# Performance work log

Measured on AMD Instinct MI355X. Metric: run time of the kernel, lower is better.

## Reference

```python
import jax, jax.numpy as jnp
import numpy as np

NEG_SLOPE = 0.2  # PyG GATConv default negative_slope


def gat_conv(x, edge_index, W, att_src, att_dst, bias):
    """PyG-style GATConv (concat heads, add_self_loops=True, eval mode).
    x: [N, F_in], edge_index: [2, E] (row 0 = src j, row 1 = dst i).
    W: [F_in, H*C], att_src/att_dst: [H, C], bias: [H*C].
    """
    N = x.shape[0]
    H, C = att_src.shape
    loops = jnp.arange(N, dtype=edge_index.dtype)
    src = jnp.concatenate([edge_index[0], loops])  # [E+N]
    dst = jnp.concatenate([edge_index[1], loops])
    h = (x @ W).reshape(N, H, C)                              # [N,H,C]
    a_src = jnp.einsum('nhc,hc->nh', h, att_src)              # [N,H]
    a_dst = jnp.einsum('nhc,hc->nh', h, att_dst)
    alpha = jax.nn.leaky_relu(a_src[src] + a_dst[dst], NEG_SLOPE)  # [E+N,H]
    # segment softmax over edges sharing the same destination node
    m = jax.ops.segment_max(alpha, dst, num_segments=N)       # [N,H]
    e = jnp.exp(alpha - jax.lax.stop_gradient(m)[dst])
    denom = jax.ops.segment_sum(e, dst, num_segments=N)       # [N,H]
    a = e / (denom[dst] + 1e-16)                              # [E+N,H]
    msg = h[src] * a[:, :, None]                              # [E+N,H,C]
    out = jax.ops.segment_sum(msg, dst, num_segments=N)       # [N,H,C]
    return out.reshape(N, H * C) + bias


def setup_inputs() -> dict:
    key = jax.random.key(0)
    ks = jax.random.split(key, 10)
    N, F, NC, C1, H1 = 50000, 128, 40, 16, 8
    E = 800000
    x = jax.random.normal(ks[0], (N, F), dtype=jnp.float32)
    edge_index = jax.random.randint(ks[1], (2, E), 0, N, dtype=jnp.int64)
    s1 = 1.0 / np.sqrt(F)
    W1 = jax.random.uniform(ks[2], (F, H1 * C1), jnp.float32, -s1, s1)
    att_src1 = jax.random.uniform(ks[3], (H1, C1), jnp.float32, -1.0, 1.0) * s1
    att_dst1 = jax.random.uniform(ks[4], (H1, C1), jnp.float32, -1.0, 1.0) * s1
    bias1 = jnp.zeros((H1 * C1,), jnp.float32)
    s2 = 1.0 / np.sqrt(H1 * C1)
    W2 = jax.random.uniform(ks[5], (H1 * C1, NC), jnp.float32, -s2, s2)
    att_src2 = jax.random.uniform(ks[6], (1, NC), jnp.float32, -1.0, 1.0) * s2
    att_dst2 = jax.random.uniform(ks[7], (1, NC), jnp.float32, -1.0, 1.0) * s2
    bias2 = jnp.zeros((NC,), jnp.float32)
    return {"x": x, "edge_index": edge_index, "W1": W1, "att_src1": att_src1,
            "att_dst1": att_dst1, "bias1": bias1, "W2": W2, "att_src2": att_src2,
            "att_dst2": att_dst2, "bias2": bias2}


def reference(x, edge_index, W1, att_src1, att_dst1, bias1, W2, att_src2, att_dst2, bias2):
    h = gat_conv(x, edge_index, W1, att_src1, att_dst1, bias1)   # [N, 128]
    # dropout in eval mode = identity
    out = gat_conv(h, edge_index, W2, att_src2, att_dst2, bias2)  # [N, 40]
    return out
```

## Files before the change

### kernel.cpp

```cpp
#include <hip/hip_runtime.h>
#include <hip/hip_bf16.h>
#include <math.h>

#define NEG_SLOPE 0.2f

typedef __bf16 bf16x8 __attribute__((ext_vector_type(8)));
typedef float f32x4 __attribute__((ext_vector_type(4)));

__device__ __forceinline__ float lrelu(float x) { return x > 0.f ? x : NEG_SLOPE * x; }

__device__ __forceinline__ unsigned short f2bfu(float f) {
    unsigned int ua = __float_as_uint(f);
    return (unsigned short)((ua + 0x7fffu + ((ua >> 16) & 1u)) >> 16);
}
__device__ __forceinline__ float bfu2f(unsigned short u) {
    return __uint_as_float(((unsigned int)u) << 16);
}
__device__ __forceinline__ float bf_lo(unsigned int u) { return __uint_as_float(u << 16); }
__device__ __forceinline__ float bf_hi(unsigned int u) { return __uint_as_float(u & 0xffff0000u); }

__global__ __launch_bounds__(256) void k_prep(const float* __restrict__ W1,
                                              bf16x8* __restrict__ Wp,
                                              const float* __restrict__ W2,
                                              bf16x8* __restrict__ W2p,
                                              int* __restrict__ cnt, int N) {
    int g = blockIdx.x * 256 + threadIdx.x;
    if (g < 2048) {
        int n = g & 15, quad = (g >> 4) & 3, c = (g >> 6) & 3, ct = g >> 8;
        bf16x8 v;
#pragma unroll
        for (int j = 0; j < 8; ++j)
            v[j] = (__bf16)W1[(c * 32 + quad * 8 + j) * 128 + ct * 16 + n];
        Wp[g] = v;
    } else if (g < 2816) {
        int idx = g - 2048;
        int n = idx & 15, quad = (idx >> 4) & 3, c = (idx >> 6) & 3, ct = idx >> 8;
        int colc = ct * 16 + n;
        bf16x8 v;
#pragma unroll
        for (int j = 0; j < 8; ++j)
            v[j] = (colc < 40) ? (__bf16)W2[(c * 32 + quad * 8 + j) * 40 + colc] : (__bf16)0.f;
        W2p[idx] = v;
    }
    if (g < N) cnt[g] = 0;
}

__global__ __launch_bounds__(256) void k_hist(const int* __restrict__ ei, int E, int N,
                                              int* __restrict__ cnt,
                                              unsigned short* __restrict__ rank) {
    int e = blockIdx.x * 256 + threadIdx.x;
    if (e >= E + N) return;
    int d = (e < E) ? ei[E + e] : (e - E);
    rank[e] = (unsigned short)atomicAdd(&cnt[d], 1);
}

__global__ __launch_bounds__(256) void k_scan_part(const int* __restrict__ cnt, int N,
                                                   int* __restrict__ psum) {
    __shared__ int sh[256];
    int t = threadIdx.x;
    int base = blockIdx.x * 1024 + t * 4;
    int tl = 0;
#pragma unroll
    for (int j = 0; j < 4; ++j) tl += (base + j < N) ? cnt[base + j] : 0;
    sh[t] = tl; __syncthreads();
    for (int off = 128; off > 0; off >>= 1) {
        if (t < off) sh[t] += sh[t + off];
        __syncthreads();
    }
    if (t == 0) psum[blockIdx.x] = sh[0];
}

__global__ __launch_bounds__(256) void k_scan_add(const int* __restrict__ cnt, int N,
                                                  const int* __restrict__ psum,
                                                  int* __restrict__ rowptr) {
    __shared__ int sh[256];
    __shared__ int basep;
    int t = threadIdx.x;
    if (t == 0) {
        int s = 0;
        for (int i = 0; i < blockIdx.x; ++i) s += psum[i];
        basep = s;
    }
    int base = blockIdx.x * 1024 + t * 4;
    int c[4]; int tl = 0;
#pragma unroll
    for (int j = 0; j < 4; ++j) { c[j] = (base + j < N) ? cnt[base + j] : 0; tl += c[j]; }
    sh[t] = tl; __syncthreads();
    for (int off = 1; off < 256; off <<= 1) {
        int a = (t >= off) ? sh[t - off] : 0;
        __syncthreads();
        sh[t] += a;
        __syncthreads();
    }
    int run = basep + (sh[t] - tl);
#pragma unroll
    for (int j = 0; j < 4; ++j) {
        if (base + j < N) { rowptr[base + j] = run; run += c[j]; }
    }
}

__global__ __launch_bounds__(256) void k_scatter(const int* __restrict__ ei, int E, int N,
                                                 const int* __restrict__ rowptr,
                                                 const unsigned short* __restrict__ rank,
                                                 unsigned short* __restrict__ col) {
    int e = blockIdx.x * 256 + threadIdx.x;
    if (e >= E + N) return;
    int s, d;
    if (e < E) { s = ei[e]; d = ei[E + e]; } else { s = d = e - E; }
    col[rowptr[d] + (int)rank[e]] = (unsigned short)s;
}

__global__ __launch_bounds__(256) void k_gemm1(const float* __restrict__ x,
                                               const bf16x8* __restrict__ Wp,
                                               const float* __restrict__ att_s,
                                               const float* __restrict__ att_d,
                                               unsigned short* __restrict__ h1A,
                                               unsigned short* __restrict__ h1B,
                                               float* __restrict__ a_src,
                                               float* __restrict__ a_dst, int N) {
    int t = threadIdx.x;
    int w = t >> 6, lane = t & 63, quad = lane >> 4, n16 = lane & 15;
    int row0 = blockIdx.x * 64 + w * 16;
    int arow = row0 + n16; if (arow >= N) arow = N - 1;
    const float* px = x + (size_t)arow * 128;

    bf16x8 ah[4], al[4];
#pragma unroll
    for (int c = 0; c < 4; ++c) {
        float4 v0 = *(const float4*)&px[c * 32 + quad * 8];
        float4 v1 = *(const float4*)&px[c * 32 + quad * 8 + 4];
        float xf[8] = {v0.x, v0.y, v0.z, v0.w, v1.x, v1.y, v1.z, v1.w};
#pragma unroll
        for (int j = 0; j < 8; ++j) {
            __bf16 hi = (__bf16)xf[j];
            ah[c][j] = hi;
            al[c][j] = (__bf16)(xf[j] - (float)hi);
        }
    }

    f32x4 acc[8];
#pragma unroll
    for (int ct = 0; ct < 8; ++ct) acc[ct] = (f32x4){0.f, 0.f, 0.f, 0.f};

    const uint4* wp4 = (const uint4*)Wp;
#pragma unroll
    for (int ct = 0; ct < 8; ++ct) {
#pragma unroll
        for (int c = 0; c < 4; ++c) {
            union { uint4 u; bf16x8 b; } bu;
            bu.u = wp4[((ct * 4 + c) * 4 + quad) * 16 + n16];
            acc[ct] = __builtin_amdgcn_mfma_f32_16x16x32_bf16(ah[c], bu.b, acc[ct], 0, 0, 0);
            acc[ct] = __builtin_amdgcn_mfma_f32_16x16x32_bf16(al[c], bu.b, acc[ct], 0, 0, 0);
        }
    }

    float asv[8], adv[8];
#pragma unroll
    for (int ct = 0; ct < 8; ++ct) {
        asv[ct] = att_s[ct * 16 + n16];
        adv[ct] = att_d[ct * 16 + n16];
    }
    int nodeb = row0 + quad * 4;
#pragma unroll
    for (int ct = 0; ct < 8; ++ct) {
        unsigned short* hp = (ct < 4) ? h1A : h1B;
        int chl = (ct & 3) * 16 + n16;
#pragma unroll
        for (int reg = 0; reg < 4; ++reg) {
            int node = nodeb + reg;
            float hv = acc[ct][reg];
            float ps = hv * asv[ct];
            float pd = hv * adv[ct];
#pragma unroll
            for (int m = 1; m < 16; m <<= 1) {
                ps += __shfl_xor(ps, m);
                pd += __shfl_xor(pd, m);
            }
            if (node < N) {
                hp[(size_t)node * 64 + chl] = f2bfu(hv);
                if (n16 == 0) {
                    a_src[(size_t)node * 8 + ct] = ps;
                    a_dst[(size_t)node * 8 + ct] = pd;
                }
            }
        }
    }
}

__global__ __launch_bounds__(256) void k_aggr1(const int* __restrict__ rowptr,
                                               const int* __restrict__ cnt,
                                               const unsigned short* __restrict__ col,
                                               const float* __restrict__ a_src,
                                               const float* __restrict__ a_dst,
                                               const unsigned int* __restrict__ h1A,
                                               const unsigned int* __restrict__ h1B,
                                               const float* __restrict__ bias1,
                                               unsigned int* __restrict__ out1h,
                                               unsigned int* __restrict__ out1l,
                                               int N, int nag) {
    __shared__ float evs[4][2][128];
    __shared__ int   cls[4][2][32];
    int p = (blockIdx.x >= nag) ? 1 : 0;
    int blk = blockIdx.x - p * nag;
    const unsigned int* hp = p ? h1B : h1A;
    int t = threadIdx.x;
    int w = t >> 6;
    int lane = t & 63;
    int half = lane >> 5;
    int u = lane & 31;
    int node = blk * 8 + w * 2 + half;
    bool nv = (node < N);
    int nodec = nv ? node : (N - 1);
    int beg = rowptr[nodec];
    int deg = nv ? cnt[nodec] : 0;
    int degO = __shfl_xor(deg, 32);
    int degmax = (deg > degO) ? deg : degO;
    if (degmax <= 0) return;

    int hh = u >> 3;
    float4 ad4 = *(const float4*)&a_dst[(size_t)nodec * 8 + p * 4];

    float* myev = &evs[w][half][0];
    int*   mycl = &cls[w][half][0];

    float den = 0.f, n0 = 0.f, n1 = 0.f;
    int c = 0;
    while (c < degmax) {
        int slot = c + u;
        int slotc = (slot < deg) ? slot : (deg - 1);
        if (slotc < 0) slotc = 0;
        int su = (int)col[beg + slotc];
        float4 as4 = *(const float4*)&a_src[(size_t)su * 8 + p * 4];
        bool valid = (slot < deg);
        float e0 = valid ? __expf(lrelu(as4.x + ad4.x)) : 0.f;
        float e1 = valid ? __expf(lrelu(as4.y + ad4.y)) : 0.f;
        float e2 = valid ? __expf(lrelu(as4.z + ad4.z)) : 0.f;
        float e3 = valid ? __expf(lrelu(as4.w + ad4.w)) : 0.f;
        *(float4*)&myev[u * 4] = make_float4(e0, e1, e2, e3);
        mycl[u] = su;

        int ccm = degmax - c; ccm = (ccm < 32) ? ccm : 32;
        int last = ccm - 1;
        int s0 = mycl[0];
        unsigned int u0 = hp[s0 * 32 + u];
        int i1 = (1 < last) ? 1 : last;
        int s1 = mycl[i1];
        unsigned int u1 = hp[s1 * 32 + u];
        int i2 = (2 < last) ? 2 : last;
        int s2 = mycl[i2];
        unsigned int u2 = hp[s2 * 32 + u];
        int body = ccm - 3;
        int i = 0;
#pragma unroll 4
        for (; i < body; ++i) {
            int sN = mycl[i + 3];
            unsigned int uN = hp[sN * 32 + u];
            float ev = myev[i * 4 + hh];
            den += ev;
            n0 = fmaf(ev, bf_lo(u0), n0);
            n1 = fmaf(ev, bf_hi(u0), n1);
            u0 = u1; u1 = u2; u2 = uN;
        }
        for (; i < ccm; ++i) {
            float ev = myev[i * 4 + hh];
            den += ev;
            n0 = fmaf(ev, bf_lo(u0), n0);
            n1 = fmaf(ev, bf_hi(u0), n1);
            u0 = u1; u1 = u2;
        }
        c += 32;
    }
    if (nv) {
        float inv = 1.f / (den + 1e-16f);
        int ch = p * 64 + 2 * u;
        float2 b = *(const float2*)&bias1[ch];
        float o0 = fmaf(n0, inv, b.x), o1 = fmaf(n1, inv, b.y);
        unsigned short h0 = f2bfu(o0), h1 = f2bfu(o1);
        float l0 = o0 - bfu2f(h0), l1 = o1 - bfu2f(h1);
        size_t idx = (size_t)node * 64 + p * 32 + u;
        out1h[idx] = (unsigned int)h0 | ((unsigned int)h1 << 16);
        out1l[idx] = (unsigned int)f2bfu(l0) | ((unsigned int)f2bfu(l1) << 16);
    }
}

__global__ __launch_bounds__(256) void k_gemm2(const unsigned int* __restrict__ out1h,
                                               const unsigned int* __restrict__ out1l,
                                               const bf16x8* __restrict__ W2p,
                                               const float* __restrict__ att_s2,
                                               const float* __restrict__ att_d2,
                                               unsigned short* __restrict__ h2s,
                                               float* __restrict__ a_src2,
                                               float* __restrict__ a_dst2, int N) {
    int t = threadIdx.x;
    int w = t >> 6, lane = t & 63, quad = lane >> 4, n16 = lane & 15;
    int row0 = blockIdx.x * 64 + w * 16;
    int arow = row0 + n16; if (arow >= N) arow = N - 1;

    bf16x8 ah[4], al[4];
#pragma unroll
    for (int c = 0; c < 4; ++c) {
        size_t base = (size_t)arow * 64 + (c * 32 + quad * 8) / 2;
        union { uint4 u; bf16x8 b; } hu, lu;
        hu.u = *(const uint4*)&out1h[base];
        lu.u = *(const uint4*)&out1l[base];
        ah[c] = hu.b;
        al[c] = lu.b;
    }

    f32x4 acc[3];
#pragma unroll
    for (int ct = 0; ct < 3; ++ct) acc[ct] = (f32x4){0.f, 0.f, 0.f, 0.f};

    const uint4* wp4 = (const uint4*)W2p;
#pragma unroll
    for (int ct = 0; ct < 3; ++ct) {
#pragma unroll
        for (int c = 0; c < 4; ++c) {
            union { uint4 u; bf16x8 b; } bu;
            bu.u = wp4[((ct * 4 + c) * 4 + quad) * 16 + n16];
            acc[ct] = __builtin_amdgcn_mfma_f32_16x16x32_bf16(ah[c], bu.b, acc[ct], 0, 0, 0);
            acc[ct] = __builtin_amdgcn_mfma_f32_16x16x32_bf16(al[c], bu.b, acc[ct], 0, 0, 0);
        }
    }

    float asv[3], adv[3];
#pragma unroll
    for (int ct = 0; ct < 3; ++ct) {
        int ch = ct * 16 + n16;
        asv[ct] = (ch < 40) ? att_s2[ch] : 0.f;
        adv[ct] = (ch < 40) ? att_d2[ch] : 0.f;
    }
    int nodeb = row0 + quad * 4;
#pragma unroll
    for (int reg = 0; reg < 4; ++reg) {
        int node = nodeb + reg;
        float ps = 0.f, pd = 0.f;
#pragma unroll
        for (int ct = 0; ct < 3; ++ct) {
            float hv = acc[ct][reg];
            ps = fmaf(hv, asv[ct], ps);
            pd = fmaf(hv, adv[ct], pd);
            int ch = ct * 16 + n16;
            if (node < N && ch < 40) h2s[(size_t)node * 64 + ch] = f2bfu(hv);
        }
#pragma unroll
        for (int m = 1; m < 16; m <<= 1) {
            ps += __shfl_xor(ps, m);
            pd += __shfl_xor(pd, m);
        }
        if (node < N && n16 == 0) {
            a_src2[node] = ps;
            a_dst2[node] = pd;
        }
    }
}

__global__ __launch_bounds__(256) void k_aggr2(const int* __restrict__ rowptr,
                                               const int* __restrict__ cnt,
                                               const unsigned short* __restrict__ col,
                                               const float* __restrict__ a_src,
                                               const float* __restrict__ a_dst,
                                               const unsigned int* __restrict__ h2b,
                                               const float* __restrict__ bias2,
                                               float* __restrict__ out, int N) {
    __shared__ float evs[4][2][32];
    __shared__ int   cls[4][2][32];
    int t = threadIdx.x;
    int w = t >> 6;
    int lane = t & 63;
    int half = lane >> 5;
    int u = lane & 31;
    int node = blockIdx.x * 8 + w * 2 + half;
    bool nv = (node < N);
    int nodec = nv ? node : (N - 1);
    int beg = rowptr[nodec];
    int deg = nv ? cnt[nodec] : 0;
    int degO = __shfl_xor(deg, 32);
    int degmax = (deg > degO) ? deg : degO;
    if (degmax <= 0) return;

    int ucl = (u < 20) ? u : 19;
    float ad = a_dst[nodec];
    float* myev = &evs[w][half][0];
    int*   mycl = &cls[w][half][0];

    float den = 0.f, a0 = 0.f, a1 = 0.f;
    int c = 0;
    while (c < degmax) {
        int slot = c + u;
        int slotc = (slot < deg) ? slot : (deg - 1);
        if (slotc < 0) slotc = 0;
        int su = (int)col[beg + slotc];
        float ev = (slot < deg) ? __expf(lrelu(a_src[su] + ad)) : 0.f;
        myev[u] = ev;
        mycl[u] = su;

        int ccm = degmax - c; ccm = (ccm < 32) ? ccm : 32;
        int last = ccm - 1;
        int s0 = mycl[0];
        unsigned int u0 = h2b[s0 * 32 + ucl];
        int i1 = (1 < last) ? 1 : last;
        int s1 = mycl[i1];
        unsigned int u1 = h2b[s1 * 32 + ucl];
        int i2 = (2 < last) ? 2 : last;
        int s2 = mycl[i2];
        unsigned int u2 = h2b[s2 * 32 + ucl];
        int body = ccm - 3;
        int i = 0;
#pragma unroll 4
        for (; i < body; ++i) {
            int sN = mycl[i + 3];
            unsigned int uN = h2b[sN * 32 + ucl];
            float evv = myev[i];
            den += evv;
            a0 = fmaf(evv, bf_lo(u0), a0);
            a1 = fmaf(evv, bf_hi(u0), a1);
            u0 = u1; u1 = u2; u2 = uN;
        }
        for (; i < ccm; ++i) {
            float evv = myev[i];
            den += evv;
            a0 = fmaf(evv, bf_lo(u0), a0);
            a1 = fmaf(evv, bf_hi(u0), a1);
            u0 = u1; u1 = u2;
        }
        c += 32;
    }
    if (nv && u < 20) {
        float inv = 1.f / (den + 1e-16f);
        float2 b = *(const float2*)&bias2[2 * u];
        float2 o = make_float2(fmaf(a0, inv, b.x), fmaf(a1, inv, b.y));
        *(float2*)&out[(size_t)node * 40 + 2 * u] = o;
    }
}

extern "C" void kernel_launch(void* const* d_in, const int* in_sizes, int n_in,
                              void* d_out, int out_size, void* d_ws, size_t ws_size,
                              hipStream_t stream) {
    const float* x   = (const float*)d_in[0];
    const int*   ei  = (const int*)d_in[1];
    const float* W1  = (const float*)d_in[2];
    const float* as1 = (const float*)d_in[3];
    const float* ad1 = (const float*)d_in[4];
    const float* b1  = (const float*)d_in[5];
    const float* W2  = (const float*)d_in[6];
    const float* as2 = (const float*)d_in[7];
    const float* ad2 = (const float*)d_in[8];
    const float* b2  = (const float*)d_in[9];

    int N = in_sizes[0] / 128;
    int E = in_sizes[1] / 2;
    int EN = E + N;
    size_t Np = (size_t)((N + 3) & ~3);
    size_t ENp = ((size_t)EN + 3) & ~3;

    float* ws = (float*)d_ws;
    unsigned int* out1h = (unsigned int*)ws; ws += Np * 64;
    unsigned int* out1l = (unsigned int*)ws; ws += Np * 64;
    unsigned int* h1A = (unsigned int*)ws; ws += Np * 32;
    unsigned int* h1Bp = (unsigned int*)ws; ws += Np * 32;
    unsigned int* h2b = (unsigned int*)ws; ws += Np * 32;
    float* a_src1  = ws; ws += Np * 8;
    float* a_dst1  = ws; ws += Np * 8;
    float* a_src2v = ws; ws += Np;
    float* a_dst2v = ws; ws += Np;
    bf16x8* Wp  = (bf16x8*)ws; ws += 2048 * 4;
    bf16x8* W2p = (bf16x8*)ws; ws += 768 * 4;
    int* cnt    = (int*)ws; ws += Np;
    int* rowptr = (int*)ws; ws += Np;
    int* psum   = (int*)ws; ws += 256;
    unsigned short* col  = (unsigned short*)ws; ws += ENp / 2 + 4;
    unsigned short* rank = (unsigned short*)ws; ws += ENp / 2 + 4;

    int nb = (N + 1023) / 1024;
    int npre = (N > 2816 ? N : 2816);

    k_prep<<<(npre + 255) / 256, 256, 0, stream>>>(W1, Wp, W2, W2p, cnt, N);
    k_hist<<<(EN + 255) / 256, 256, 0, stream>>>(ei, E, N, cnt, rank);
    k_scan_part<<<nb, 256, 0, stream>>>(cnt, N, psum);
    k_scan_add<<<nb, 256, 0, stream>>>(cnt, N, psum, rowptr);
    k_scatter<<<(EN + 255) / 256, 256, 0, stream>>>(ei, E, N, rowptr, rank, col);

    k_gemm1<<<(N + 63) / 64, 256, 0, stream>>>(x, Wp, as1, ad1,
                                               (unsigned short*)h1A, (unsigned short*)h1Bp,
                                               a_src1, a_dst1, N);
    int nag = (N + 7) / 8;
    k_aggr1<<<2 * nag, 256, 0, stream>>>(rowptr, cnt, col, a_src1, a_dst1,
                                         h1A, h1Bp, b1, out1h, out1l, N, nag);
    k_gemm2<<<(N + 63) / 64, 256, 0, stream>>>(out1h, out1l, W2p, as2, ad2,
                                               (unsigned short*)h2b, a_src2v, a_dst2v, N);
    k_aggr2<<<nag, 256, 0, stream>>>(rowptr, cnt, col, a_src2v, a_dst2v, h2b, b2, (float*)d_out, N);
}
```

Before: 238.0 us.

## Gather neighbor rows with 16-byte loads, four edges per wave-half step

Both aggregation kernels now have each lane load a uint4 (eight bf16 channels) of a neighbor row, with four groups of 8 lanes covering four edges at once. Before, each lane loaded one 32-bit word per edge. Partial sums are combined across the edge groups with xor shuffles, and results are written with vector stores. The aim is fewer, wider gather instructions and fewer serial loop iterations per node. In exchange it uses more registers (eight accumulators plus four uint4 prefetch buffers) and adds a shuffle reduction at the end.

```diff
diff --git a/kernel.cpp b/kernel.cpp
--- a/kernel.cpp
+++ b/kernel.cpp
@@ -202,12 +202,15 @@
     __shared__ int   cls[4][2][32];
     int p = (blockIdx.x >= nag) ? 1 : 0;
     int blk = blockIdx.x - p * nag;
-    const unsigned int* hp = p ? h1B : h1A;
+    const uint4* hp4 = (const uint4*)(p ? h1B : h1A);
     int t = threadIdx.x;
     int w = t >> 6;
     int lane = t & 63;
     int half = lane >> 5;
     int u = lane & 31;
+    int e4 = u >> 3;
+    int v  = u & 7;
+    int hh = v >> 1;
     int node = blk * 8 + w * 2 + half;
     bool nv = (node < N);
     int nodec = nv ? node : (N - 1);
@@ -217,13 +220,15 @@
     int degmax = (deg > degO) ? deg : degO;
     if (degmax <= 0) return;
 
-    int hh = u >> 3;
     float4 ad4 = *(const float4*)&a_dst[(size_t)nodec * 8 + p * 4];
-
     float* myev = &evs[w][half][0];
     int*   mycl = &cls[w][half][0];
 
-    float den = 0.f, n0 = 0.f, n1 = 0.f;
+    float den = 0.f;
+    float nm[8];
+#pragma unroll
+    for (int k = 0; k < 8; ++k) nm[k] = 0.f;
+
     int c = 0;
     while (c < degmax) {
         int slot = c + u;
@@ -240,46 +245,72 @@
         mycl[u] = su;
 
         int ccm = degmax - c; ccm = (ccm < 32) ? ccm : 32;
-        int last = ccm - 1;
-        int s0 = mycl[0];
-        unsigned int u0 = hp[s0 * 32 + u];
-        int i1 = (1 < last) ? 1 : last;
-        int s1 = mycl[i1];
-        unsigned int u1 = hp[s1 * 32 + u];
-        int i2 = (2 < last) ? 2 : last;
-        int s2 = mycl[i2];
-        unsigned int u2 = hp[s2 * 32 + u];
-        int body = ccm - 3;
-        int i = 0;
-#pragma unroll 4
-        for (; i < body; ++i) {
-            int sN = mycl[i + 3];
-            unsigned int uN = hp[sN * 32 + u];
-            float ev = myev[i * 4 + hh];
+        int ng = (ccm + 3) >> 2;
+        int gl = ng - 1;
+        int g1 = (1 < gl) ? 1 : gl;
+        int g2 = (2 < gl) ? 2 : gl;
+        int g3 = (3 < gl) ? 3 : gl;
+        uint4 U0 = hp4[mycl[e4] * 8 + v];
+        uint4 U1 = hp4[mycl[g1 * 4 + e4] * 8 + v];
+        uint4 U2 = hp4[mycl[g2 * 4 + e4] * 8 + v];
+        uint4 U3 = hp4[mycl[g3 * 4 + e4] * 8 + v];
+        int body = ng - 4;
+        int g = 0;
+#pragma unroll 2
+        for (; g < body; ++g) {
+            uint4 UN = hp4[mycl[(g + 4) * 4 + e4] * 8 + v];
+            float ev = myev[(g * 4 + e4) * 4 + hh];
             den += ev;
-            n0 = fmaf(ev, bf_lo(u0), n0);
-            n1 = fmaf(ev, bf_hi(u0), n1);
-            u0 = u1; u1 = u2; u2 = uN;
-        }
-        for (; i < ccm; ++i) {
-            float ev = myev[i * 4 + hh];
+            nm[0] = fmaf(ev, bf_lo(U0.x), nm[0]);
+            nm[1] = fmaf(ev, bf_hi(U0.x), nm[1]);
+            nm[2] = fmaf(ev, bf_lo(U0.y), nm[2]);
+            nm[3] = fmaf(ev, bf_hi(U0.y), nm[3]);
+            nm[4] = fmaf(ev, bf_lo(U0.z), nm[4]);
+            nm[5] = fmaf(ev, bf_hi(U0.z), nm[5]);
+            nm[6] = fmaf(ev, bf_lo(U0.w), nm[6]);
+            nm[7] = fmaf(ev, bf_hi(U0.w), nm[7]);
+            U0 = U1; U1 = U2; U2 = U3; U3 = UN;
+        }
+        for (; g < ng; ++g) {
+            float ev = myev[(g * 4 + e4) * 4 + hh];
             den += ev;
-            n0 = fmaf(ev, bf_lo(u0), n0);
-            n1 = fmaf(ev, bf_hi(u0), n1);
-            u0 = u1; u1 = u2;
+            nm[0] = fmaf(ev, bf_lo(U0.x), nm[0]);
+            nm[1] = fmaf(ev, bf_hi(U0.x), nm[1]);
+            nm[2] = fmaf(ev, bf_lo(U0.y), nm[2]);
+            nm[3] = fmaf(ev, bf_hi(U0.y), nm[3]);
+            nm[4] = fmaf(ev, bf_lo(U0.z), nm[4]);
+            nm[5] = fmaf(ev, bf_hi(U0.z), nm[5]);
+            nm[6] = fmaf(ev, bf_lo(U0.w), nm[6]);
+            nm[7] = fmaf(ev, bf_hi(U0.w), nm[7]);
+            U0 = U1; U1 = U2; U2 = U3;
         }
         c += 32;
     }
-    if (nv) {
+    den += __shfl_xor(den, 8);
+    den += __shfl_xor(den, 16);
+#pragma unroll
+    for (int k = 0; k < 8; ++k) {
+        nm[k] += __shfl_xor(nm[k], 8);
+        nm[k] += __shfl_xor(nm[k], 16);
+    }
+    if (nv && e4 == 0) {
         float inv = 1.f / (den + 1e-16f);
-        int ch = p * 64 + 2 * u;
-        float2 b = *(const float2*)&bias1[ch];
-        float o0 = fmaf(n0, inv, b.x), o1 = fmaf(n1, inv, b.y);
-        unsigned short h0 = f2bfu(o0), h1 = f2bfu(o1);
-        float l0 = o0 - bfu2f(h0), l1 = o1 - bfu2f(h1);
-        size_t idx = (size_t)node * 64 + p * 32 + u;
-        out1h[idx] = (unsigned int)h0 | ((unsigned int)h1 << 16);
-        out1l[idx] = (unsigned int)f2bfu(l0) | ((unsigned int)f2bfu(l1) << 16);
+        float4 b0 = *(const float4*)&bias1[p * 64 + v * 8];
+        float4 b1 = *(const float4*)&bias1[p * 64 + v * 8 + 4];
+        float bb[8] = {b0.x, b0.y, b0.z, b0.w, b1.x, b1.y, b1.z, b1.w};
+        unsigned int H[4], L[4];
+#pragma unroll
+        for (int q = 0; q < 4; ++q) {
+            float o0 = fmaf(nm[2 * q],     inv, bb[2 * q]);
+            float o1 = fmaf(nm[2 * q + 1], inv, bb[2 * q + 1]);
+            unsigned short h0 = f2bfu(o0), h1 = f2bfu(o1);
+            float l0 = o0 - bfu2f(h0), l1 = o1 - bfu2f(h1);
+            H[q] = (unsigned int)h0 | ((unsigned int)h1 << 16);
+            L[q] = (unsigned int)f2bfu(l0) | ((unsigned int)f2bfu(l1) << 16);
+        }
+        size_t idx = (size_t)node * 64 + p * 32 + v * 4;
+        *(uint4*)&out1h[idx] = make_uint4(H[0], H[1], H[2], H[3]);
+        *(uint4*)&out1l[idx] = make_uint4(L[0], L[1], L[2], L[3]);
     }
 }
 
@@ -370,6 +401,8 @@
     int lane = t & 63;
     int half = lane >> 5;
     int u = lane & 31;
+    int e4 = u >> 3;
+    int v  = u & 7;
     int node = blockIdx.x * 8 + w * 2 + half;
     bool nv = (node < N);
     int nodec = nv ? node : (N - 1);
@@ -379,12 +412,16 @@
     int degmax = (deg > degO) ? deg : degO;
     if (degmax <= 0) return;
 
-    int ucl = (u < 20) ? u : 19;
+    const uint4* h24 = (const uint4*)h2b;
     float ad = a_dst[nodec];
     float* myev = &evs[w][half][0];
     int*   mycl = &cls[w][half][0];
 
-    float den = 0.f, a0 = 0.f, a1 = 0.f;
+    float den = 0.f;
+    float am[8];
+#pragma unroll
+    for (int k = 0; k < 8; ++k) am[k] = 0.f;
+
     int c = 0;
     while (c < degmax) {
         int slot = c + u;
@@ -396,41 +433,65 @@
         mycl[u] = su;
 
         int ccm = degmax - c; ccm = (ccm < 32) ? ccm : 32;
-        int last = ccm - 1;
-        int s0 = mycl[0];
-        unsigned int u0 = h2b[s0 * 32 + ucl];
-        int i1 = (1 < last) ? 1 : last;
-        int s1 = mycl[i1];
-        unsigned int u1 = h2b[s1 * 32 + ucl];
-        int i2 = (2 < last) ? 2 : last;
-        int s2 = mycl[i2];
-        unsigned int u2 = h2b[s2 * 32 + ucl];
-        int body = ccm - 3;
-        int i = 0;
-#pragma unroll 4
-        for (; i < body; ++i) {
-            int sN = mycl[i + 3];
-            unsigned int uN = h2b[sN * 32 + ucl];
-            float evv = myev[i];
+        int ng = (ccm + 3) >> 2;
+        int gl = ng - 1;
+        int g1 = (1 < gl) ? 1 : gl;
+        int g2 = (2 < gl) ? 2 : gl;
+        int g3 = (3 < gl) ? 3 : gl;
+        uint4 U0 = h24[mycl[e4] * 8 + v];
+        uint4 U1 = h24[mycl[g1 * 4 + e4] * 8 + v];
+        uint4 U2 = h24[mycl[g2 * 4 + e4] * 8 + v];
+        uint4 U3 = h24[mycl[g3 * 4 + e4] * 8 + v];
+        int body = ng - 4;
+        int g = 0;
+#pragma unroll 2
+        for (; g < body; ++g) {
+            uint4 UN = h24[mycl[(g + 4) * 4 + e4] * 8 + v];
+            float evv = myev[g * 4 + e4];
             den += evv;
-            a0 = fmaf(evv, bf_lo(u0), a0);
-            a1 = fmaf(evv, bf_hi(u0), a1);
-            u0 = u1; u1 = u2; u2 = uN;
-        }
-        for (; i < ccm; ++i) {
-            float evv = myev[i];
+            am[0] = fmaf(evv, bf_lo(U0.x), am[0]);
+            am[1] = fmaf(evv, bf_hi(U0.x), am[1]);
+            am[2] = fmaf(evv, bf_lo(U0.y), am[2]);
+            am[3] = fmaf(evv, bf_hi(U0.y), am[3]);
+            am[4] = fmaf(evv, bf_lo(U0.z), am[4]);
+            am[5] = fmaf(evv, bf_hi(U0.z), am[5]);
+            am[6] = fmaf(evv, bf_lo(U0.w), am[6]);
+            am[7] = fmaf(evv, bf_hi(U0.w), am[7]);
+            U0 = U1; U1 = U2; U2 = U3; U3 = UN;
+        }
+        for (; g < ng; ++g) {
+            float evv = myev[g * 4 + e4];
             den += evv;
-            a0 = fmaf(evv, bf_lo(u0), a0);
-            a1 = fmaf(evv, bf_hi(u0), a1);
-            u0 = u1; u1 = u2;
+            am[0] = fmaf(evv, bf_lo(U0.x), am[0]);
+            am[1] = fmaf(evv, bf_hi(U0.x), am[1]);
+            am[2] = fmaf(evv, bf_lo(U0.y), am[2]);
+            am[3] = fmaf(evv, bf_hi(U0.y), am[3]);
+            am[4] = fmaf(evv, bf_lo(U0.z), am[4]);
+            am[5] = fmaf(evv, bf_hi(U0.z), am[5]);
+            am[6] = fmaf(evv, bf_lo(U0.w), am[6]);
+            am[7] = fmaf(evv, bf_hi(U0.w), am[7]);
+            U0 = U1; U1 = U2; U2 = U3;
         }
         c += 32;
     }
-    if (nv && u < 20) {
+    den += __shfl_xor(den, 8);
+    den += __shfl_xor(den, 16);
+#pragma unroll
+    for (int k = 0; k < 8; ++k) {
+        am[k] += __shfl_xor(am[k], 8);
+        am[k] += __shfl_xor(am[k], 16);
+    }
+    if (nv && e4 == 0 && v < 5) {
         float inv = 1.f / (den + 1e-16f);
-        float2 b = *(const float2*)&bias2[2 * u];
-        float2 o = make_float2(fmaf(a0, inv, b.x), fmaf(a1, inv, b.y));
-        *(float2*)&out[(size_t)node * 40 + 2 * u] = o;
+        float4 b0 = *(const float4*)&bias2[v * 8];
+        float4 b1 = *(const float4*)&bias2[v * 8 + 4];
+        float4 o0 = make_float4(fmaf(am[0], inv, b0.x), fmaf(am[1], inv, b0.y),
+                                fmaf(am[2], inv, b0.z), fmaf(am[3], inv, b0.w));
+        float4 o1 = make_float4(fmaf(am[4], inv, b1.x), fmaf(am[5], inv, b1.y),
+                                fmaf(am[6], inv, b1.z), fmaf(am[7], inv, b1.w));
+        size_t ob = (size_t)node * 40 + v * 8;
+        *(float4*)&out[ob] = o0;
+        *(float4*)&out[ob + 4] = o1;
     }
 }
 
```

Measured after the change: 232.6 us. -2.3%, faster.
